# Optimization experiments

Hardware: AMD Instinct MI355X
Metric: run time of the kernel (lower is better)

The kernel has to match this reference:

```python
import jax, jax.numpy as jnp
import numpy as np

V, C, L, D = 50000, 125000, 500000, 128


def _l2norm(x):
    n = jnp.sqrt(jnp.sum(x * x, axis=-1, keepdims=True))
    return x / jnp.maximum(n, 1e-12)


def _combine(x, W1, b1, W2, b2):
    # SymmetricSumCombine element op: normalize(sigmoid(layer1(x)) + layer2(x));
    # the outer sum over set members is done by segment_sum by the caller.
    return _l2norm(jax.nn.sigmoid(x @ W1 + b1) + (x @ W2 + b2))


def setup_inputs() -> dict:
    key = jax.random.key(0)
    ks = jax.random.split(key, 22)
    s = 1.0 / np.sqrt(D)
    w = lambda k: jax.random.normal(k, (D, D), jnp.float32) * s
    b = lambda k: jax.random.normal(k, (D,), jnp.float32) * s
    return {
        "variables": jax.random.normal(ks[0], (V, D), jnp.float32),
        "lit_var": jax.random.randint(ks[1], (L,), 0, V, jnp.int32),
        "lit_sign": jax.random.randint(ks[2], (L,), 0, 2, jnp.int32),
        "lit_clause": jnp.sort(jax.random.randint(ks[3], (L,), 0, C, jnp.int32)),
        "clause_var": jax.random.randint(ks[4], (C,), 0, V, jnp.int32),
        "neg_W": w(ks[5]), "neg_b": b(ks[6]),
        "vc_W1": w(ks[7]), "vc_b1": b(ks[8]), "vc_W2": w(ks[9]), "vc_b2": b(ks[10]),
        "cc_W1": w(ks[11]), "cc_b1": b(ks[12]), "cc_W2": w(ks[13]), "cc_b2": b(ks[14]),
        "W_z": w(ks[15]), "U_z": w(ks[16]), "W_r": w(ks[17]), "U_r": w(ks[18]),
        "W_h": w(ks[19]), "U_h": w(ks[20]),
    }


def reference(variables, lit_var, lit_sign, lit_clause, clause_var,
              neg_W, neg_b, vc_W1, vc_b1, vc_W2, vc_b2,
              cc_W1, cc_b1, cc_W2, cc_b2,
              W_z, U_z, W_r, U_r, W_h, U_h):
    n_vars = variables.shape[0]
    n_clauses = clause_var.shape[0]
    # gather per-literal variable embeddings, negate negative literals
    v = variables[lit_var]  # [L, D]
    v = jnp.where((lit_sign > 0)[:, None], v @ neg_W + neg_b, v)
    # variable_combiner per literal, summed into clause embeddings
    t = _combine(v, vc_W1, vc_b1, vc_W2, vc_b2)  # [L, D]
    ce = jax.ops.segment_sum(t, lit_clause, num_segments=n_clauses)  # [C, D]
    # clause_combiner per clause, summed into owner variable message
    c = _combine(ce, cc_W1, cc_b1, cc_W2, cc_b2)  # [C, D]
    av = jax.ops.segment_sum(c, clause_var, num_segments=n_vars)  # [V, D]
    # variables with no clauses keep their own embedding as the message
    cnt = jnp.zeros((n_vars,), jnp.float32).at[clause_var].add(1.0)
    av = jnp.where((cnt > 0)[:, None], av, variables)
    # GRU update
    z = jax.nn.sigmoid(av @ W_z + variables @ U_z)
    r = jax.nn.sigmoid(av @ W_r + variables @ U_r)
    h_tilda = jnp.tanh(av @ W_h + (r * variables) @ U_h)
    return (1.0 - z) * variables + z * h_tilda
```

## Files before the change

### kernel.cpp

```cpp
#include <hip/hip_runtime.h>

#define V_N 50000
#define C_N 125000
#define L_N 500000
#define NCH2 31250

typedef __attribute__((ext_vector_type(8))) short short8;
typedef __attribute__((ext_vector_type(4))) float f32x4;

__device__ inline unsigned short f2bf(float f) {
  union { float f; unsigned u; } v; v.f = f;
  unsigned r = v.u + 0x7FFFu + ((v.u >> 16) & 1u);
  return (unsigned short)(r >> 16);
}
__device__ inline float bf2f(unsigned short h) {
  union { unsigned u; float f; } v; v.u = ((unsigned)h) << 16;
  return v.f;
}
__device__ inline float sigm(float x) { return 1.f / (1.f + __expf(-x)); }

struct WPtrs { const float* w[11]; };

__global__ __launch_bounds__(256) void k_front(
    WPtrs p, unsigned short* __restrict__ wt,
    const int* __restrict__ lit_var, const int* __restrict__ lit_sign,
    const int* __restrict__ lit_clause, int* __restrict__ pmeta,
    int* __restrict__ bnd, const int* __restrict__ clause_var,
    int* __restrict__ cnt, int* __restrict__ dst) {
  int b = blockIdx.x;
  if (b < 704) {
    int idx = b * 256 + threadIdx.x;
    int m = idx >> 14;
    int j = idx & 16383;
    int k = j >> 7, col = j & 127;
    float val = p.w[m][j];
    int chunk = ((col >> 5) << 3) + (((col >> 4) & 1) << 2) + (k >> 5);
    int off = (((k >> 3) & 3) << 7) + ((col & 15) << 3) + (k & 7);
    wt[m * 16384 + chunk * 512 + off] = f2bf(val);
  } else if (b < 2658) {
    int i = (b - 704) * 256 + threadIdx.x;
    if (i < L_N)
      pmeta[i] = lit_var[i] | (lit_sign[i] << 16) | ((lit_clause[i] & 63) << 17);
  } else if (b < 2781) {
    int i = (b - 2658) * 256 + threadIdx.x;
    if (i <= NCH2) {
      int key = i * 4;
      int lo = 0, hi = L_N;
      while (lo < hi) {
        int mid = (lo + hi) >> 1;
        if (lit_clause[mid] < key) lo = mid + 1; else hi = mid;
      }
      bnd[i] = lo;
    }
  } else {
    int i = (b - 2781) * 256 + threadIdx.x;
    if (i < C_N) {
      int v = clause_var[i];
      dst[i] = atomicAdd(&cnt[v], 1);
    }
  }
}

__device__ inline void load_bfrags(const unsigned short* __restrict__ Wt,
                                   short8 B[2][4], int wave, int lane) {
#pragma unroll
  for (int ct = 0; ct < 2; ++ct)
#pragma unroll
    for (int ks = 0; ks < 4; ++ks)
      B[ct][ks] = *(const short8*)(Wt + (((wave << 3) + (ct << 2) + ks) << 9) +
                                   (lane << 3));
}

__device__ inline void gemm_reg(const unsigned short (*__restrict__ xs)[136],
                                const short8 B[2][4], f32x4 acc[4][2], int lane) {
  const int lan15 = lane & 15, kq = lane >> 4;
#pragma unroll
  for (int ks = 0; ks < 4; ++ks) {
#pragma unroll
    for (int rt = 0; rt < 4; ++rt) {
      short8 a = *(const short8*)(&xs[rt * 16 + lan15][ks * 32 + kq * 8]);
#pragma unroll
      for (int ct = 0; ct < 2; ++ct)
        acc[rt][ct] = __builtin_amdgcn_mfma_f32_16x16x32_bf16(a, B[ct][ks], acc[rt][ct], 0, 0, 0);
    }
  }
}

__device__ inline void zero_acc(f32x4 acc[4][2]) {
#pragma unroll
  for (int rt = 0; rt < 4; ++rt)
#pragma unroll
    for (int ct = 0; ct < 2; ++ct) acc[rt][ct] = (f32x4)(0.f);
}

__device__ inline void gemm_reg32(const unsigned short (*__restrict__ xs)[136],
                                  const short8 B[2][4], f32x4 acc[2][2], int lane) {
  const int lan15 = lane & 15, kq = lane >> 4;
#pragma unroll
  for (int ks = 0; ks < 4; ++ks) {
#pragma unroll
    for (int rt = 0; rt < 2; ++rt) {
      short8 a = *(const short8*)(&xs[rt * 16 + lan15][ks * 32 + kq * 8]);
#pragma unroll
      for (int ct = 0; ct < 2; ++ct)
        acc[rt][ct] = __builtin_amdgcn_mfma_f32_16x16x32_bf16(a, B[ct][ks], acc[rt][ct], 0, 0, 0);
    }
  }
}

__device__ inline void zero_acc2(f32x4 acc[2][2]) {
#pragma unroll
  for (int rt = 0; rt < 2; ++rt)
#pragma unroll
    for (int ct = 0; ct < 2; ++ct) acc[rt][ct] = (f32x4)(0.f);
}

__device__ inline void stage_f32_32(const float* __restrict__ base, long vb, int nrows,
                                    unsigned short (*__restrict__ dst)[136], int tid) {
  int r = tid >> 3, cq = (tid & 7) * 16;
  long v = vb + r;
  bool valid = v < nrows;
  const float* src = valid ? base + v * 128 : base;
#pragma unroll
  for (int j = 0; j < 16; j += 4) {
    float4 x4 = *(const float4*)(src + cq + j);
    if (!valid) { x4.x = 0.f; x4.y = 0.f; x4.z = 0.f; x4.w = 0.f; }
    dst[r][cq + j + 0] = f2bf(x4.x);
    dst[r][cq + j + 1] = f2bf(x4.y);
    dst[r][cq + j + 2] = f2bf(x4.z);
    dst[r][cq + j + 3] = f2bf(x4.w);
  }
}

__global__ __launch_bounds__(256, 2) void k_tables(
    const float* __restrict__ vars,
    const unsigned short* __restrict__ negWt, const float* __restrict__ negb,
    const unsigned short* __restrict__ W1t, const float* __restrict__ b1,
    const unsigned short* __restrict__ W2t, const float* __restrict__ b2,
    unsigned short* __restrict__ t_pos, unsigned short* __restrict__ t_neg) {
  __shared__ unsigned short xs[32][136];
  __shared__ unsigned short ys[32][136];
  __shared__ float ssp[32][4];
  const int tid = threadIdx.x;
  const int wave = tid >> 6, lane = tid & 63;
  const int lan15 = lane & 15, kq = lane >> 4;
  const long vb = (long)blockIdx.x * 32;

  stage_f32_32(vars, vb, V_N, xs, tid);
  __syncthreads();

  float nb[2], bb1[2], bb2[2];
#pragma unroll
  for (int ct = 0; ct < 2; ++ct) {
    int col = wave * 32 + ct * 16 + lan15;
    nb[ct] = negb[col]; bb1[ct] = b1[col]; bb2[ct] = b2[col];
  }
  {
    short8 BN[2][4];
    load_bfrags(negWt, BN, wave, lane);
    f32x4 acc[2][2];
    zero_acc2(acc);
    gemm_reg32(xs, BN, acc, lane);
#pragma unroll
    for (int rt = 0; rt < 2; ++rt)
#pragma unroll
      for (int ct = 0; ct < 2; ++ct) {
        int col = wave * 32 + ct * 16 + lan15;
#pragma unroll
        for (int reg = 0; reg < 4; ++reg)
          ys[rt * 16 + kq * 4 + reg][col] = f2bf(acc[rt][ct][reg] + nb[ct]);
      }
  }
  __syncthreads();

  short8 B1f[2][4], B2f[2][4];
  load_bfrags(W1t, B1f, wave, lane);
  load_bfrags(W2t, B2f, wave, lane);

#pragma unroll
  for (int pass = 0; pass < 2; ++pass) {
    const unsigned short (*A)[136] = pass ? ys : xs;
    unsigned short* dst = pass ? t_neg : t_pos;
    f32x4 a1[2][2], a2[2][2];
    zero_acc2(a1); zero_acc2(a2);
    gemm_reg32(A, B1f, a1, lane);
    gemm_reg32(A, B2f, a2, lane);
    float s[2][2][4]; float ss[2][4];
#pragma unroll
    for (int rt = 0; rt < 2; ++rt) {
#pragma unroll
      for (int reg = 0; reg < 4; ++reg) ss[rt][reg] = 0.f;
#pragma unroll
      for (int ct = 0; ct < 2; ++ct)
#pragma unroll
        for (int reg = 0; reg < 4; ++reg) {
          float v = sigm(a1[rt][ct][reg] + bb1[ct]) + (a2[rt][ct][reg] + bb2[ct]);
          s[rt][ct][reg] = v; ss[rt][reg] += v * v;
        }
    }
#pragma unroll
    for (int rt = 0; rt < 2; ++rt)
#pragma unroll
      for (int reg = 0; reg < 4; ++reg) {
        float v = ss[rt][reg];
        v += __shfl_xor(v, 1); v += __shfl_xor(v, 2);
        v += __shfl_xor(v, 4); v += __shfl_xor(v, 8);
        if (lan15 == 0) ssp[rt * 16 + kq * 4 + reg][wave] = v;
      }
    __syncthreads();
#pragma unroll
    for (int rt = 0; rt < 2; ++rt)
#pragma unroll
      for (int reg = 0; reg < 4; ++reg) {
        int row = rt * 16 + kq * 4 + reg;
        float tot = ssp[row][0] + ssp[row][1] + ssp[row][2] + ssp[row][3];
        float inv = 1.f / fmaxf(sqrtf(tot), 1e-12f);
        long vr = vb + row;
        if (vr < V_N) {
#pragma unroll
          for (int ct = 0; ct < 2; ++ct)
            dst[vr * 128 + wave * 32 + ct * 16 + lan15] = f2bf(s[rt][ct][reg] * inv);
        }
      }
    __syncthreads();
  }
}

__global__ __launch_bounds__(256) void k_scan_pre(const int* __restrict__ cnt,
                                                  int* __restrict__ bsum) {
  __shared__ int sh[256];
  const int tid = threadIdx.x;
  int i = blockIdx.x * 256 + tid;
  int v = (i < V_N) ? cnt[i] : 0;
  sh[tid] = v;
  __syncthreads();
  for (int off = 1; off < 256; off <<= 1) {
    int add = (tid >= off) ? sh[tid - off] : 0;
    __syncthreads();
    sh[tid] += add;
    __syncthreads();
  }
  if (tid == 255) bsum[blockIdx.x] = sh[255];
}

__global__ __launch_bounds__(256) void k_scan_post(const int* __restrict__ cnt,
                                                   const int* __restrict__ bsum,
                                                   int* __restrict__ col_start,
                                                   int nb) {
  __shared__ int sh[256];
  __shared__ int shb[256];
  const int tid = threadIdx.x;
  int bv = (tid < nb) ? bsum[tid] : 0;
  shb[tid] = bv;
  __syncthreads();
  for (int off = 1; off < 256; off <<= 1) {
    int add = (tid >= off) ? shb[tid - off] : 0;
    __syncthreads();
    shb[tid] += add;
    __syncthreads();
  }
  int bpref = (blockIdx.x == 0) ? 0 : shb[blockIdx.x - 1];
  int i = blockIdx.x * 256 + tid;
  int v = (i < V_N) ? cnt[i] : 0;
  sh[tid] = v;
  __syncthreads();
  for (int off = 1; off < 256; off <<= 1) {
    int add = (tid >= off) ? sh[tid - off] : 0;
    __syncthreads();
    sh[tid] += add;
    __syncthreads();
  }
  if (i < V_N) col_start[i + 1] = sh[tid] + bpref;
  if (i == 0) col_start[0] = 0;
}

__global__ __launch_bounds__(256, 2) void k_sc_clause(
    const int* __restrict__ pmeta, const int* __restrict__ bnd,
    const unsigned short* __restrict__ t_pos,
    const unsigned short* __restrict__ t_neg,
    const int* __restrict__ dst, const int* __restrict__ col_start,
    const int* __restrict__ clause_var,
    const unsigned short* __restrict__ W1t, const float* __restrict__ b1,
    const unsigned short* __restrict__ W2t, const float* __restrict__ b2,
    unsigned short* __restrict__ crows) {
  __shared__ unsigned short xs[64][136];
  __shared__ float ssp[64][4];
  __shared__ int dsts[64];
  const int tid = threadIdx.x;
  const int wave = tid >> 6, lane = tid & 63;
  const int lan15 = lane & 15, kq = lane >> 4;
  const int cb = blockIdx.x * 64;

  if (tid < 64) {
    int c = cb + tid;
    dsts[tid] = (c < C_N) ? dst[c] + col_start[clause_var[c]] : -1;
  }

  int bi0 = blockIdx.x * 16 + wave * 4;
  int i0 = bi0 < NCH2 ? bi0 : NCH2;
  int i1 = (bi0 + 4) < NCH2 ? (bi0 + 4) : NCH2;
  int ws = bnd[i0], we = bnd[i1];

  f32x4 acc[8];
#pragma unroll
  for (int s = 0; s < 8; ++s) acc[s] = (f32x4)(0.f);

  const int mtarget = wave * 16 + lan15;

  for (int base = ws; base < we; base += 32) {
    int mm = 0x00FE0000;
    if (lane < 32) {
      int idx = base + lane;
      if (idx < we) mm = pmeta[idx];
    }
    unsigned au[4];
#pragma unroll
    for (int pp = 0; pp < 4; ++pp) {
      int m0 = __shfl(mm, 8 * kq + 2 * pp);
      int m1 = __shfl(mm, 8 * kq + 2 * pp + 1);
      unsigned lo = (((m0 >> 17) & 127) == mtarget) ? 0x3F80u : 0u;
      unsigned hi = (((m1 >> 17) & 127) == mtarget) ? 0x3F800000u : 0u;
      au[pp] = lo | hi;
    }
    unsigned t16[8][8];
#pragma unroll
    for (int e = 0; e < 8; ++e) {
      int mv = __shfl(mm, 8 * kq + e);
      int v = mv & 0xFFFF;
      const unsigned short* rp =
          ((mv & 0x10000) ? t_neg : t_pos) + (long)v * 128 + lan15;
#pragma unroll
      for (int s = 0; s < 8; ++s) t16[e][s] = rp[s * 16];
    }
    union { unsigned u[4]; short8 s8; } ua;
    ua.u[0] = au[0]; ua.u[1] = au[1]; ua.u[2] = au[2]; ua.u[3] = au[3];
#pragma unroll
    for (int s = 0; s < 8; ++s) {
      union { unsigned u[4]; short8 s8; } ub;
#pragma unroll
      for (int d = 0; d < 4; ++d)
        ub.u[d] = t16[2 * d][s] | (t16[2 * d + 1][s] << 16);
      acc[s] = __builtin_amdgcn_mfma_f32_16x16x32_bf16(ua.s8, ub.s8, acc[s], 0, 0, 0);
    }
  }

#pragma unroll
  for (int s = 0; s < 8; ++s)
#pragma unroll
    for (int reg = 0; reg < 4; ++reg)
      xs[wave * 16 + 4 * kq + reg][s * 16 + lan15] = f2bf(acc[s][reg]);
  __syncthreads();

  short8 B1f[2][4], B2f[2][4];
  load_bfrags(W1t, B1f, wave, lane);
  load_bfrags(W2t, B2f, wave, lane);
  float bb1[2], bb2[2];
#pragma unroll
  for (int ct = 0; ct < 2; ++ct) {
    int col = wave * 32 + ct * 16 + lan15;
    bb1[ct] = b1[col]; bb2[ct] = b2[col];
  }
  f32x4 a1[4][2], a2[4][2];
  zero_acc(a1); zero_acc(a2);
  gemm_reg(xs, B1f, a1, lane);
  gemm_reg(xs, B2f, a2, lane);
  float s[4][2][4]; float ss[4][4];
#pragma unroll
  for (int rt = 0; rt < 4; ++rt) {
#pragma unroll
    for (int reg = 0; reg < 4; ++reg) ss[rt][reg] = 0.f;
#pragma unroll
    for (int ct = 0; ct < 2; ++ct)
#pragma unroll
      for (int reg = 0; reg < 4; ++reg) {
        float v = sigm(a1[rt][ct][reg] + bb1[ct]) + (a2[rt][ct][reg] + bb2[ct]);
        s[rt][ct][reg] = v; ss[rt][reg] += v * v;
      }
  }
#pragma unroll
  for (int rt = 0; rt < 4; ++rt)
#pragma unroll
    for (int reg = 0; reg < 4; ++reg) {
      float v = ss[rt][reg];
      v += __shfl_xor(v, 1); v += __shfl_xor(v, 2);
      v += __shfl_xor(v, 4); v += __shfl_xor(v, 8);
      if (lan15 == 0) ssp[rt * 16 + kq * 4 + reg][wave] = v;
    }
  __syncthreads();
#pragma unroll
  for (int rt = 0; rt < 4; ++rt)
#pragma unroll
    for (int reg = 0; reg < 4; ++reg) {
      int row = rt * 16 + kq * 4 + reg;
      float tot = ssp[row][0] + ssp[row][1] + ssp[row][2] + ssp[row][3];
      float inv = 1.f / fmaxf(sqrtf(tot), 1e-12f);
      int dd = dsts[row];
      if (dd >= 0) {
#pragma unroll
        for (int ct = 0; ct < 2; ++ct)
          crows[(long)dd * 128 + wave * 32 + ct * 16 + lan15] =
              f2bf(s[rt][ct][reg] * inv);
      }
    }
}

__global__ __launch_bounds__(256, 2) void k_gru(
    const float* __restrict__ vars,
    const unsigned short* __restrict__ crows, const int* __restrict__ col_start,
    const unsigned short* __restrict__ Wzt, const unsigned short* __restrict__ Uzt,
    const unsigned short* __restrict__ Wrt, const unsigned short* __restrict__ Urt,
    const unsigned short* __restrict__ Wht, const unsigned short* __restrict__ Uht,
    float* __restrict__ out) {
  __shared__ unsigned short as_[32][136];
  __shared__ unsigned short vs[32][136];
  const int tid = threadIdx.x;
  const int wave = tid >> 6, lane = tid & 63;
  const int lan15 = lane & 15, kq = lane >> 4;
  const long vb = (long)blockIdx.x * 32;

  {
    int r = tid >> 3, cq = (tid & 7) * 16;
    long v = vb + r;
    if (v < V_N) {
      int s0 = col_start[v], s1 = col_start[v + 1];
      if (s1 > s0) {
        float acc[16];
#pragma unroll
        for (int j = 0; j < 16; ++j) acc[j] = 0.f;
        for (int t = s0; t < s1; ++t) {
          const unsigned short* rp = crows + (long)t * 128 + cq;
#pragma unroll
          for (int j = 0; j < 16; j += 8) {
            short8 u = *(const short8*)(rp + j);
#pragma unroll
            for (int e = 0; e < 8; ++e) acc[j + e] += bf2f((unsigned short)u[e]);
          }
        }
#pragma unroll
        for (int j = 0; j < 16; ++j) as_[r][cq + j] = f2bf(acc[j]);
      } else {
#pragma unroll
        for (int j = 0; j < 16; j += 4) {
          float4 x4 = *(const float4*)(vars + v * 128 + cq + j);
          as_[r][cq + j + 0] = f2bf(x4.x);
          as_[r][cq + j + 1] = f2bf(x4.y);
          as_[r][cq + j + 2] = f2bf(x4.z);
          as_[r][cq + j + 3] = f2bf(x4.w);
        }
      }
    } else {
#pragma unroll
      for (int j = 0; j < 16; ++j) as_[r][cq + j] = 0;
    }
  }
  stage_f32_32(vars, vb, V_N, vs, tid);
  __syncthreads();

  f32x4 az[2][2];
  zero_acc2(az);
  {
    short8 BA[2][4], BB[2][4];
    load_bfrags(Wzt, BA, wave, lane);
    load_bfrags(Uzt, BB, wave, lane);
    gemm_reg32(as_, BA, az, lane);
    gemm_reg32(vs, BB, az, lane);
  }
  f32x4 ar[2][2];
  zero_acc2(ar);
  {
    short8 BA[2][4], BB[2][4];
    load_bfrags(Wrt, BA, wave, lane);
    load_bfrags(Urt, BB, wave, lane);
    gemm_reg32(as_, BA, ar, lane);
    gemm_reg32(vs, BB, ar, lane);
  }
  __syncthreads();
#pragma unroll
  for (int rt = 0; rt < 2; ++rt)
#pragma unroll
    for (int ct = 0; ct < 2; ++ct) {
      int col = wave * 32 + ct * 16 + lan15;
#pragma unroll
      for (int reg = 0; reg < 4; ++reg) {
        int row = rt * 16 + kq * 4 + reg;
        float rr = sigm(ar[rt][ct][reg]);
        float vf = bf2f(vs[row][col]);
        vs[row][col] = f2bf(rr * vf);
      }
    }
  __syncthreads();
  f32x4 ah[2][2];
  zero_acc2(ah);
  {
    short8 BA[2][4], BB[2][4];
    load_bfrags(Wht, BA, wave, lane);
    load_bfrags(Uht, BB, wave, lane);
    gemm_reg32(as_, BA, ah, lane);
    gemm_reg32(vs, BB, ah, lane);
  }
#pragma unroll
  for (int rt = 0; rt < 2; ++rt)
#pragma unroll
    for (int ct = 0; ct < 2; ++ct) {
      int col = wave * 32 + ct * 16 + lan15;
#pragma unroll
      for (int reg = 0; reg < 4; ++reg) {
        int row = rt * 16 + kq * 4 + reg;
        long v = vb + row;
        if (v < V_N) {
          float z = sigm(az[rt][ct][reg]);
          float h = tanhf(ah[rt][ct][reg]);
          float vf = vars[v * 128 + col];
          out[v * 128 + col] = (1.f - z) * vf + z * h;
        }
      }
    }
}

extern "C" void kernel_launch(void* const* d_in, const int* in_sizes, int n_in,
                              void* d_out, int out_size, void* d_ws, size_t ws_size,
                              hipStream_t stream) {
  const float* vars = (const float*)d_in[0];
  const int* lit_var = (const int*)d_in[1];
  const int* lit_sign = (const int*)d_in[2];
  const int* lit_clause = (const int*)d_in[3];
  const int* clause_var = (const int*)d_in[4];
  const float* negW = (const float*)d_in[5];
  const float* negb = (const float*)d_in[6];
  const float* vcW1 = (const float*)d_in[7];
  const float* vcb1 = (const float*)d_in[8];
  const float* vcW2 = (const float*)d_in[9];
  const float* vcb2 = (const float*)d_in[10];
  const float* ccW1 = (const float*)d_in[11];
  const float* ccb1 = (const float*)d_in[12];
  const float* ccW2 = (const float*)d_in[13];
  const float* ccb2 = (const float*)d_in[14];
  const float* Wz = (const float*)d_in[15];
  const float* Uz = (const float*)d_in[16];
  const float* Wr = (const float*)d_in[17];
  const float* Ur = (const float*)d_in[18];
  const float* Wh = (const float*)d_in[19];
  const float* Uh = (const float*)d_in[20];

  unsigned char* ws = (unsigned char*)d_ws;
  unsigned short* wt = (unsigned short*)ws;
  unsigned short* t_pos = (unsigned short*)(ws + 360448);
  unsigned short* t_neg = (unsigned short*)(ws + 13160448);
  unsigned short* crows = (unsigned short*)(ws + 25960448);
  int* col_start = (int*)(ws + 58000000);
  int* cnt = (int*)(ws + 58300000);
  int* dst = (int*)(ws + 58600000);
  int* bsum = (int*)(ws + 59200000);
  int* bnd = (int*)(ws + 59300000);
  int* pmeta = (int*)(ws + 59500000);
  if (ws_size < (size_t)61500000) return;

  const int NB = (V_N + 255) / 256;

  WPtrs p;
  p.w[0] = negW; p.w[1] = vcW1; p.w[2] = vcW2; p.w[3] = ccW1; p.w[4] = ccW2;
  p.w[5] = Wz; p.w[6] = Uz; p.w[7] = Wr; p.w[8] = Ur; p.w[9] = Wh; p.w[10] = Uh;

  hipMemsetAsync(ws + 58300000, 0, (size_t)200000, stream);
  hipLaunchKernelGGL(k_front, dim3(3270), dim3(256), 0, stream, p, wt,
                     lit_var, lit_sign, lit_clause, pmeta, bnd, clause_var,
                     cnt, dst);

  hipLaunchKernelGGL(k_scan_pre, dim3(NB), dim3(256), 0, stream, cnt, bsum);
  hipLaunchKernelGGL(k_scan_post, dim3(NB), dim3(256), 0, stream, cnt, bsum,
                     col_start, NB);

  hipLaunchKernelGGL(k_tables, dim3((V_N + 31) / 32), dim3(256), 0, stream,
                     vars, wt + 0, negb, wt + 16384, vcb1, wt + 2 * 16384, vcb2,
                     t_pos, t_neg);

  hipLaunchKernelGGL(k_sc_clause, dim3((C_N + 63) / 64), dim3(256), 0, stream,
                     pmeta, bnd, t_pos, t_neg, dst, col_start, clause_var,
                     wt + 3 * 16384, ccb1, wt + 4 * 16384, ccb2, crows);

  hipLaunchKernelGGL(k_gru, dim3((V_N + 31) / 32), dim3(256), 0, stream,
                     vars, crows, col_start,
                     wt + 5 * 16384, wt + 6 * 16384, wt + 7 * 16384,
                     wt + 8 * 16384, wt + 9 * 16384, wt + 10 * 16384,
                     (float*)d_out);
}
```

Baseline: 146.3 us.

## Stage gathered literal rows through LDS with vector loads in clause scatter kernel

Replaces the per-lane scalar 2-byte global gathers of literal rows (64 loads per lane per step) with coalesced 16-byte loads into a per-wave LDS staging area. The MFMA B fragments are then read back from LDS. The shared buffer is enlarged to hold the staging area and reused as xs, and the occupancy hint is raised from 2 to 4 blocks. The intent is fewer, wider global memory transactions. The cost is extra LDS traffic, and correctness relies on an inline waitcnt with no barrier, since each wave only touches its own region.

```diff
diff --git a/kernel.cpp b/kernel.cpp
--- a/kernel.cpp
+++ b/kernel.cpp
@@ -274,7 +274,7 @@
   if (i == 0) col_start[0] = 0;
 }
 
-__global__ __launch_bounds__(256, 2) void k_sc_clause(
+__global__ __launch_bounds__(256, 4) void k_sc_clause(
     const int* __restrict__ pmeta, const int* __restrict__ bnd,
     const unsigned short* __restrict__ t_pos,
     const unsigned short* __restrict__ t_neg,
@@ -283,9 +283,10 @@
     const unsigned short* __restrict__ W1t, const float* __restrict__ b1,
     const unsigned short* __restrict__ W2t, const float* __restrict__ b2,
     unsigned short* __restrict__ crows) {
-  __shared__ unsigned short xs[64][136];
+  __shared__ __align__(16) unsigned char smem[35328];
   __shared__ float ssp[64][4];
   __shared__ int dsts[64];
+  unsigned short (*xs)[136] = (unsigned short (*)[136])smem;
   const int tid = threadIdx.x;
   const int wave = tid >> 6, lane = tid & 63;
   const int lan15 = lane & 15, kq = lane >> 4;
@@ -306,12 +307,25 @@
   for (int s = 0; s < 8; ++s) acc[s] = (f32x4)(0.f);
 
   const int mtarget = wave * 16 + lan15;
+  const int srow = lane >> 4, schunk = lane & 15;
+  unsigned char* const wbase = smem + wave * 8832;
+  const unsigned short* const rbase =
+      (const unsigned short*)(wbase + kq * 2208 + lan15 * 2);
 
   for (int base = ws; base < we; base += 32) {
     int mm = 0x00FE0000;
     if (lane < 32) {
       int idx = base + lane;
       if (idx < we) mm = pmeta[idx];
+    }
+#pragma unroll
+    for (int p = 0; p < 8; ++p) {
+      int r = p * 4 + srow;
+      int mv = __shfl(mm, r);
+      int v = mv & 0xFFFF;
+      const unsigned short* tb = (mv & 0x10000) ? t_neg : t_pos;
+      uint4 u = *(const uint4*)(tb + (long)v * 128 + schunk * 8);
+      *(uint4*)(wbase + (r >> 3) * 2208 + (r & 7) * 272 + schunk * 16) = u;
     }
     unsigned au[4];
 #pragma unroll
@@ -322,27 +336,27 @@
       unsigned hi = (((m1 >> 17) & 127) == mtarget) ? 0x3F800000u : 0u;
       au[pp] = lo | hi;
     }
-    unsigned t16[8][8];
-#pragma unroll
-    for (int e = 0; e < 8; ++e) {
-      int mv = __shfl(mm, 8 * kq + e);
-      int v = mv & 0xFFFF;
-      const unsigned short* rp =
-          ((mv & 0x10000) ? t_neg : t_pos) + (long)v * 128 + lan15;
-#pragma unroll
-      for (int s = 0; s < 8; ++s) t16[e][s] = rp[s * 16];
-    }
     union { unsigned u[4]; short8 s8; } ua;
     ua.u[0] = au[0]; ua.u[1] = au[1]; ua.u[2] = au[2]; ua.u[3] = au[3];
+
+    asm volatile("s_waitcnt lgkmcnt(0)" ::: "memory");
+
 #pragma unroll
     for (int s = 0; s < 8; ++s) {
       union { unsigned u[4]; short8 s8; } ub;
 #pragma unroll
-      for (int d = 0; d < 4; ++d)
-        ub.u[d] = t16[2 * d][s] | (t16[2 * d + 1][s] << 16);
+      for (int d = 0; d < 4; ++d) {
+        unsigned lo = *(const unsigned short*)((const unsigned char*)rbase +
+                                               (2 * d) * 272 + s * 32);
+        unsigned hi = *(const unsigned short*)((const unsigned char*)rbase +
+                                               (2 * d + 1) * 272 + s * 32);
+        ub.u[d] = lo | (hi << 16);
+      }
       acc[s] = __builtin_amdgcn_mfma_f32_16x16x32_bf16(ua.s8, ub.s8, acc[s], 0, 0, 0);
     }
   }
+
+  __syncthreads();
 
 #pragma unroll
   for (int s = 0; s < 8; ++s)
```

Result: faster. 143.4 us (-2.0%).
